# Performance work log

Measured on AMD Instinct MI355X. Metric: run time of the kernel, lower is better.

## Reference

```python
import jax, jax.numpy as jnp
import numpy as np

B, T, N, H = 32, 512, 32, 128  # batch, time, num_series (== num_chans), hidden


def setup_inputs() -> dict:
    key = jax.random.key(0)
    ks = jax.random.split(key, 7)
    s = 1.0 / np.sqrt(H)  # PyTorch LSTM default init range
    X = jax.random.normal(ks[0], (B, T, N), dtype=jnp.float32)
    W_ih = jax.random.uniform(ks[1], (N, 4 * H, N), minval=-s, maxval=s, dtype=jnp.float32)
    W_hh = jax.random.uniform(ks[2], (N, 4 * H, H), minval=-s, maxval=s, dtype=jnp.float32)
    b_ih = jax.random.uniform(ks[3], (N, 4 * H), minval=-s, maxval=s, dtype=jnp.float32)
    b_hh = jax.random.uniform(ks[4], (N, 4 * H), minval=-s, maxval=s, dtype=jnp.float32)
    W_out = jax.random.uniform(ks[5], (N, H), minval=-s, maxval=s, dtype=jnp.float32)  # Conv1d(hidden,1,1) weight per series
    b_out = jax.random.uniform(ks[6], (N,), minval=-s, maxval=s, dtype=jnp.float32)
    return dict(X=X, W_ih=W_ih, W_hh=W_hh, b_ih=b_ih, b_hh=b_hh, W_out=W_out, b_out=b_out)


def reference(X, W_ih, W_hh, b_ih, b_hh, W_out, b_out):
    """Ensemble of N independent single-layer LSTMs over the same input X,
    each followed by a 1x1 conv (linear) head; outputs concatenated on dim 2.
    Gate order follows PyTorch: i, f, g, o."""
    Bsz, Tlen, P = X.shape
    Nser, _, Hid = W_hh.shape
    # Precompute input projections for all series/timesteps: [T, N, B, 4H]
    xproj = jnp.einsum('btp,ngp->tnbg', X, W_ih) + (b_ih + b_hh)[None, :, None, :]
    h0 = jnp.zeros((Nser, Bsz, Hid), X.dtype)
    c0 = jnp.zeros((Nser, Bsz, Hid), X.dtype)

    def step(carry, xt):
        h, c = carry
        gates = xt + jnp.einsum('nbh,ngh->nbg', h, W_hh)  # [N,B,4H]
        i, f, g, o = jnp.split(gates, 4, axis=-1)
        c = jax.nn.sigmoid(f) * c + jax.nn.sigmoid(i) * jnp.tanh(g)
        h = jax.nn.sigmoid(o) * jnp.tanh(c)
        return (h, c), h

    (hT, cT), hs = jax.lax.scan(step, (h0, c0), xproj)  # hs: [T, N, B, H]
    # 1x1 conv head per series, then concatenate along series dim -> [B, T, N]
    pred = jnp.einsum('tnbh,nh->btn', hs, W_out) + b_out[None, None, :]
    return pred, hT, cT
```

## Files before the change

### kernel.cpp

```cpp
#include <hip/hip_runtime.h>
#include <hip/hip_bf16.h>

typedef __attribute__((ext_vector_type(8))) short s16x8;
typedef __attribute__((ext_vector_type(4))) float f32x4;

#define MFMA_B16(a, b, c) __builtin_amdgcn_mfma_f32_16x16x32_bf16((a), (b), (c), 0, 0, 0)

static __device__ __forceinline__ short f2bf(float f) {
    __hip_bfloat16 h = __float2bfloat16(f);
    return __builtin_bit_cast(short, h);
}
static __device__ __forceinline__ float rcp_f(float x) {
    return __builtin_amdgcn_rcpf(x);
}

__global__ void xcvt_kernel(const float* __restrict__ X, short* __restrict__ Xb, int n) {
    int i = (blockIdx.x * 256 + threadIdx.x) * 4;
    if (i < n) {
        float4 v = *(const float4*)(X + i);
        short4 o;
        o.x = f2bf(v.x); o.y = f2bf(v.y); o.z = f2bf(v.z); o.w = f2bf(v.w);
        *(short4*)(Xb + i) = o;
    }
}

template<bool BF16X>
__global__ __launch_bounds__(512, 2)
void clstm_kernel(const float* __restrict__ X,
                  const short* __restrict__ Xb,
                  const float* __restrict__ W_ih,
                  const float* __restrict__ W_hh,
                  const float* __restrict__ b_ih,
                  const float* __restrict__ b_hh,
                  const float* __restrict__ W_out,
                  const float* __restrict__ b_out,
                  float* __restrict__ out)
{
    constexpr int B = 32, T = 512, N = 32, H = 128, G = 512;
    constexpr int HT_OFF = B * T * N;
    constexpr int CT_OFF = HT_OFF + N * B * H;
    constexpr int PRED_OFF = 8192;
    constexpr float C1 = 1.4426950408889634f;

    __shared__ __align__(16) unsigned char smem[16384];

    const int tid  = threadIdx.x;
    const int w    = tid >> 6;
    const int L    = tid & 63;
    const int col  = L & 15;
    const int quad = L >> 4;
    const int n    = blockIdx.x & 31;
    const int bgrp = blockIdx.x >> 5;

    s16x8 Bh[4][4];
    s16x8 Bx[4];
    f32x4 biasv[4];
#pragma unroll
    for (int tt = 0; tt < 4; ++tt) {
        const int g = (w + 8 * tt) * 16 + col;
        const float* whr = W_hh + ((size_t)n * G + g) * H + quad * 8;
#pragma unroll
        for (int kt = 0; kt < 4; ++kt) {
            const float* p = whr + kt * 32;
#pragma unroll
            for (int jj = 0; jj < 8; ++jj) Bh[tt][kt][jj] = f2bf(p[jj]);
        }
        const float* wir = W_ih + ((size_t)n * G + g) * N + quad * 8;
#pragma unroll
        for (int jj = 0; jj < 8; ++jj) Bx[tt][jj] = f2bf(wir[jj]);
        const float bb = b_ih[n * G + g] + b_hh[n * G + g];
        biasv[tt] = (f32x4){bb, bb, bb, bb};
    }

    s16x8 Bp[4];
    const float bo = b_out[n];
    const f32x4 bov = (f32x4){bo, bo, bo, bo};
#pragma unroll
    for (int kt = 0; kt < 4; ++kt) {
        const float* wp = W_out + n * H + kt * 32 + quad * 8;
#pragma unroll
        for (int jj = 0; jj < 8; ++jj)
            Bp[kt][jj] = (col == 0) ? f2bf(wp[jj]) : (short)0;
    }

    int wboff;
    {
        const int j = w * 16 + col;
        wboff = (j >> 5) * 1024 + (((((j >> 3) & 3) << 4) | (quad << 2)) * 16) + (j & 7) * 2;
    }

    const bool xactive = (col & 3) == 0;
    const int  xb      = bgrp * 4 + (col >> 2);
    const float* xp  = X + ((size_t)xb * T) * N + quad * 8;
    const short* xbp = BF16X ? (Xb + ((size_t)xb * T) * N + quad * 8) : nullptr;

    auto loadx = [&](int t) -> s16x8 {
        s16x8 r = (s16x8)(short)0;
        if (xactive) {
            if constexpr (BF16X) {
                r = *(const s16x8*)(xbp + (size_t)t * N);
            } else {
                float4 lo = *(const float4*)(xp + (size_t)t * N);
                float4 hi = *(const float4*)(xp + (size_t)t * N + 4);
                r[0] = f2bf(lo.x); r[1] = f2bf(lo.y); r[2] = f2bf(lo.z); r[3] = f2bf(lo.w);
                r[4] = f2bf(hi.x); r[5] = f2bf(hi.y); r[6] = f2bf(hi.z); r[7] = f2bf(hi.w);
            }
        }
        return r;
    };

    *(float4*)(smem + tid * 16)        = make_float4(0.f, 0.f, 0.f, 0.f);
    *(float4*)(smem + 8192 + tid * 16) = make_float4(0.f, 0.f, 0.f, 0.f);

    float cst = 0.f, hlast = 0.f;

    f32x4 accN[4];
    {
        s16x8 x0 = loadx(0);
#pragma unroll
        for (int tt = 0; tt < 4; ++tt)
            accN[tt] = MFMA_B16(x0, Bx[tt], biasv[tt]);
    }
    s16x8 xA = loadx(1);
    s16x8 xB = loadx(2);

    __syncthreads();

#define STEP(P, TCUR)                                                               \
    {                                                                               \
        const unsigned char* rb = smem + (P) * 4096;                                \
        s16x8 Af[4];                                                                \
        _Pragma("unroll")                                                           \
        for (int kt = 0; kt < 4; ++kt)                                              \
            Af[kt] = *(const s16x8*)(rb + kt * 1024 + L * 16);                      \
        f32x4 acc[4];                                                               \
        _Pragma("unroll")                                                           \
        for (int tt = 0; tt < 4; ++tt) acc[tt] = accN[tt];                          \
        _Pragma("unroll")                                                           \
        for (int kt = 0; kt < 4; ++kt) {                                            \
            _Pragma("unroll")                                                       \
            for (int tt = 0; tt < 4; ++tt)                                          \
                acc[tt] = MFMA_B16(Af[kt], Bh[tt][kt], acc[tt]);                    \
        }                                                                           \
        if (w == ((TCUR) & 7)) {                                                    \
            f32x4 pacc = bov;                                                       \
            _Pragma("unroll")                                                       \
            for (int kt = 0; kt < 4; ++kt)                                          \
                pacc = MFMA_B16(Af[kt], Bp[kt], pacc);                              \
            if ((TCUR) > 0 && col == 0)                                             \
                *(float*)(smem + PRED_OFF + ((quad << 9) + (TCUR) - 1) * 4) =       \
                    pacc[0];                                                        \
        }                                                                           \
                         \
        _Pragma("unroll")                                                           \
        for (int tt = 0; tt < 4; ++tt)                                              \
            accN[tt] = MFMA_B16(xA, Bx[tt], biasv[tt]);                             \
        xA = xB;                                                                    \
        xB = loadx(((TCUR) + 3 < T) ? (TCUR) + 3 : T - 1);                          \
                                     \
        {                                                                           \
            const float iv = acc[0][0], fv = acc[1][0];                             \
            const float gv = acc[2][0], ov = acc[3][0];                             \
            const float ei = exp2f(-C1 * iv);                                       \
            const float ef = exp2f(-C1 * fv);                                       \
            const float eg = exp2f(-2.0f * C1 * gv);                                \
            const float eo = exp2f(-C1 * ov);                                       \
            const float sf = rcp_f(1.0f + ef);                                      \
            const float itg = (1.0f - eg) * rcp_f((1.0f + ei) * (1.0f + eg));       \
            const float cc = __builtin_fmaf(sf, cst, itg);                          \
            cst = cc;                                                               \
            const float ec = exp2f(-2.0f * C1 * cc);                                \
            const float hv = (1.0f - ec) * rcp_f((1.0f + eo) * (1.0f + ec));        \
            hlast = hv;                                                             \
            *(short*)(smem + ((P) ^ 1) * 4096 + wboff) = f2bf(hv);                  \
        }                                                                           \
        __syncthreads();                                                            \
    }

#pragma unroll 1
    for (int t2 = 0; t2 < T; t2 += 2) {
        STEP(0, t2)
        STEP(1, t2 + 1)
    }
#undef STEP

    if (w == 0) {
        f32x4 pacc = bov;
#pragma unroll
        for (int kt = 0; kt < 4; ++kt) {
            s16x8 Af = *(const s16x8*)(smem + kt * 1024 + L * 16);
            pacc = MFMA_B16(Af, Bp[kt], pacc);
        }
        if (col == 0)
            *(float*)(smem + PRED_OFF + ((quad << 9) + (T - 1)) * 4) = pacc[0];
    }
    __syncthreads();

#pragma unroll
    for (int e = tid; e < 4 * T; e += 512) {
        const int b = e >> 9, t = e & (T - 1);
        out[((size_t)(bgrp * 4 + b) * T + t) * N + n] =
            *(const float*)(smem + PRED_OFF + e * 4);
    }

    {
        const int bglob = bgrp * 4 + quad;
        const int j = w * 16 + col;
        out[HT_OFF + ((size_t)n * B + bglob) * H + j] = hlast;
        out[CT_OFF + ((size_t)n * B + bglob) * H + j] = cst;
    }
}

extern "C" void kernel_launch(void* const* d_in, const int* in_sizes, int n_in,
                              void* d_out, int out_size, void* d_ws, size_t ws_size,
                              hipStream_t stream) {
    const float* X     = (const float*)d_in[0];
    const float* W_ih  = (const float*)d_in[1];
    const float* W_hh  = (const float*)d_in[2];
    const float* b_ih  = (const float*)d_in[3];
    const float* b_hh  = (const float*)d_in[4];
    const float* W_out = (const float*)d_in[5];
    const float* b_out = (const float*)d_in[6];
    float* out = (float*)d_out;

    const int xelems = 32 * 512 * 32;
    const bool usebf = ws_size >= (size_t)xelems * sizeof(short);

    if (usebf) {
        short* Xb = (short*)d_ws;
        xcvt_kernel<<<dim3(xelems / 1024), dim3(256), 0, stream>>>(X, Xb, xelems);
        clstm_kernel<true><<<dim3(256), dim3(512), 0, stream>>>(
            X, Xb, W_ih, W_hh, b_ih, b_hh, W_out, b_out, out);
    } else {
        clstm_kernel<false><<<dim3(256), dim3(512), 0, stream>>>(
            X, nullptr, W_ih, W_hh, b_ih, b_hh, W_out, b_out, out);
    }
}
```

Baseline: 366.3 us.

## Batch input projection MFMA across four timesteps per group

Previously each step issued four MFMAs for the input projection where only a quarter of lanes carried real x data. Now all lanes load x for one of four consecutive timesteps, so one set of four MFMAs per 4-step group yields projections for all four steps, each extracted per lane from an accumulator element. This removes three quarters of the input-projection MFMAs and x loads from the serial recurrence. In exchange it relies on the MFMA output layout mapping column lanes to timesteps correctly, broadcasts a scalar into the accumulator, and adds some register pressure.

Measured after the change: 355.7 us. 2.9% less time.

```diff
diff --git a/kernel.cpp b/kernel.cpp
--- a/kernel.cpp
+++ b/kernel.cpp
@@ -89,24 +89,22 @@
         wboff = (j >> 5) * 1024 + (((((j >> 3) & 3) << 4) | (quad << 2)) * 16) + (j & 7) * 2;
     }
 
-    const bool xactive = (col & 3) == 0;
-    const int  xb      = bgrp * 4 + (col >> 2);
-    const float* xp  = X + ((size_t)xb * T) * N + quad * 8;
-    const short* xbp = BF16X ? (Xb + ((size_t)xb * T) * N + quad * 8) : nullptr;
-
-    auto loadx = [&](int t) -> s16x8 {
-        s16x8 r = (s16x8)(short)0;
-        if (xactive) {
-            if constexpr (BF16X) {
-                r = *(const s16x8*)(xbp + (size_t)t * N);
-            } else {
-                float4 lo = *(const float4*)(xp + (size_t)t * N);
-                float4 hi = *(const float4*)(xp + (size_t)t * N + 4);
-                r[0] = f2bf(lo.x); r[1] = f2bf(lo.y); r[2] = f2bf(lo.z); r[3] = f2bf(lo.w);
-                r[4] = f2bf(hi.x); r[5] = f2bf(hi.y); r[6] = f2bf(hi.z); r[7] = f2bf(hi.w);
-            }
+    const int xb = bgrp * 4 + (col >> 2);
+    const int ts = col & 3;
+    const float* xp  = X + ((size_t)xb * T + ts) * N + quad * 8;
+    const short* xbp = BF16X ? (Xb + ((size_t)xb * T + ts) * N + quad * 8) : nullptr;
+
+    auto loadxg = [&](int tg) -> s16x8 {
+        if constexpr (BF16X) {
+            return *(const s16x8*)(xbp + (size_t)tg * N);
+        } else {
+            float4 lo = *(const float4*)(xp + (size_t)tg * N);
+            float4 hi = *(const float4*)(xp + (size_t)tg * N + 4);
+            s16x8 r;
+            r[0] = f2bf(lo.x); r[1] = f2bf(lo.y); r[2] = f2bf(lo.z); r[3] = f2bf(lo.w);
+            r[4] = f2bf(hi.x); r[5] = f2bf(hi.y); r[6] = f2bf(hi.z); r[7] = f2bf(hi.w);
+            return r;
         }
-        return r;
     };
 
     *(float4*)(smem + tid * 16)        = make_float4(0.f, 0.f, 0.f, 0.f);
@@ -114,33 +112,29 @@
 
     float cst = 0.f, hlast = 0.f;
 
-    f32x4 accN[4];
-    {
-        s16x8 x0 = loadx(0);
-#pragma unroll
-        for (int tt = 0; tt < 4; ++tt)
-            accN[tt] = MFMA_B16(x0, Bx[tt], biasv[tt]);
-    }
-    s16x8 xA = loadx(1);
-    s16x8 xB = loadx(2);
+    s16x8 xgC = loadxg(0);
+    s16x8 xgN = loadxg(4);
 
     __syncthreads();
 
-#define STEP(P, TCUR)                                                               \
+#define STEP(P, TCUR, J)                                                            \
     {                                                                               \
         const unsigned char* rb = smem + (P) * 4096;                                \
         s16x8 Af[4];                                                                \
         _Pragma("unroll")                                                           \
         for (int kt = 0; kt < 4; ++kt)                                              \
             Af[kt] = *(const s16x8*)(rb + kt * 1024 + L * 16);                      \
-        f32x4 acc[4];                                                               \
+        f32x4 cur[4];                                                               \
         _Pragma("unroll")                                                           \
-        for (int tt = 0; tt < 4; ++tt) acc[tt] = accN[tt];                          \
+        for (int tt = 0; tt < 4; ++tt) {                                            \
+            const float a = acc4[tt][(J)];                                          \
+            cur[tt] = (f32x4){a, a, a, a};                                          \
+        }                                                                           \
         _Pragma("unroll")                                                           \
         for (int kt = 0; kt < 4; ++kt) {                                            \
             _Pragma("unroll")                                                       \
             for (int tt = 0; tt < 4; ++tt)                                          \
-                acc[tt] = MFMA_B16(Af[kt], Bh[tt][kt], acc[tt]);                    \
+                cur[tt] = MFMA_B16(Af[kt], Bh[tt][kt], cur[tt]);                    \
         }                                                                           \
         if (w == ((TCUR) & 7)) {                                                    \
             f32x4 pacc = bov;                                                       \
@@ -151,16 +145,10 @@
                 *(float*)(smem + PRED_OFF + ((quad << 9) + (TCUR) - 1) * 4) =       \
                     pacc[0];                                                        \
         }                                                                           \
-                         \
-        _Pragma("unroll")                                                           \
-        for (int tt = 0; tt < 4; ++tt)                                              \
-            accN[tt] = MFMA_B16(xA, Bx[tt], biasv[tt]);                             \
-        xA = xB;                                                                    \
-        xB = loadx(((TCUR) + 3 < T) ? (TCUR) + 3 : T - 1);                          \
                                      \
         {                                                                           \
-            const float iv = acc[0][0], fv = acc[1][0];                             \
-            const float gv = acc[2][0], ov = acc[3][0];                             \
+            const float iv = cur[0][0], fv = cur[1][0];                             \
+            const float gv = cur[2][0], ov = cur[3][0];                             \
             const float ei = exp2f(-C1 * iv);                                       \
             const float ef = exp2f(-C1 * fv);                                       \
             const float eg = exp2f(-2.0f * C1 * gv);                                \
@@ -178,9 +166,17 @@
     }
 
 #pragma unroll 1
-    for (int t2 = 0; t2 < T; t2 += 2) {
-        STEP(0, t2)
-        STEP(1, t2 + 1)
+    for (int tg = 0; tg < T; tg += 4) {
+        f32x4 acc4[4];
+#pragma unroll
+        for (int tt = 0; tt < 4; ++tt)
+            acc4[tt] = MFMA_B16(xgC, Bx[tt], biasv[tt]);
+        xgC = xgN;
+        xgN = loadxg((tg + 8 < T) ? (tg + 8) : (T - 4));
+        STEP(0, tg + 0, 0)
+        STEP(1, tg + 1, 1)
+        STEP(0, tg + 2, 2)
+        STEP(1, tg + 3, 3)
     }
 #undef STEP
 
```
